# Kernel tuning notes

Measured on AMD Instinct MI355X. Metric: run time of the kernel, lower is better.

Reference implementation:

```python
import jax, jax.numpy as jnp
import numpy as np

NEG_SLOPE = 0.2  # PyG GATConv default leaky_relu slope
EPS = 1e-16


def gat_conv(x, src, dst, W, att_src, att_dst, bias, heads, concat):
    """PyG-style GATConv. x: [N, Fin]; W: [Fin, heads*C]; att_*: [heads, C].
    Edge (src j -> dst i): alpha_ij = softmax_i(leaky_relu(a_src.h_j + a_dst.h_i)).
    """
    N = x.shape[0]
    h = (x @ W).reshape(N, heads, -1)                       # [N, H, C]
    a_s = jnp.einsum('nhc,hc->nh', h, att_src)              # [N, H]
    a_d = jnp.einsum('nhc,hc->nh', h, att_dst)              # [N, H]
    e = jax.nn.leaky_relu(a_s[src] + a_d[dst], NEG_SLOPE)   # [E, H]
    # numerically stable segment softmax over incoming edges of each dst node
    e_max = jax.ops.segment_max(e, dst, num_segments=N)     # [N, H]
    e_max = jnp.where(jnp.isfinite(e_max), e_max, 0.0)      # isolated nodes
    ex = jnp.exp(e - e_max[dst])                            # [E, H]
    denom = jax.ops.segment_sum(ex, dst, num_segments=N)    # [N, H]
    alpha = ex / (denom[dst] + EPS)                         # [E, H]
    msg = alpha[:, :, None] * h[src]                        # [E, H, C]
    out = jax.ops.segment_sum(msg, dst, num_segments=N)     # [N, H, C]
    out = out.reshape(N, -1) if concat else out.mean(axis=1)
    return out + bias


def setup_inputs() -> dict:
    key = jax.random.key(0)
    ks = jax.random.split(key, 12)
    N, E = 100000, 1600000
    Fin, hidden, heads, Fout = 128, 128, 8, 64
    C1 = hidden // heads  # 16
    s = lambda f: 1.0 / np.sqrt(f)
    x = jax.random.normal(ks[0], (N, Fin), dtype=jnp.float32)
    edge_index = jax.random.randint(ks[1], (2, E), 0, N, dtype=jnp.int64)
    W1 = jax.random.normal(ks[2], (Fin, heads * C1), dtype=jnp.float32) * s(Fin)
    att_src1 = jax.random.normal(ks[3], (heads, C1), dtype=jnp.float32) * s(C1)
    att_dst1 = jax.random.normal(ks[4], (heads, C1), dtype=jnp.float32) * s(C1)
    b1 = jnp.zeros((hidden,), dtype=jnp.float32)
    W2 = jax.random.normal(ks[5], (hidden, Fout), dtype=jnp.float32) * s(hidden)
    att_src2 = jax.random.normal(ks[6], (1, Fout), dtype=jnp.float32) * s(Fout)
    att_dst2 = jax.random.normal(ks[7], (1, Fout), dtype=jnp.float32) * s(Fout)
    b2 = jnp.zeros((Fout,), dtype=jnp.float32)
    return {"x": x, "edge_index": edge_index,
            "W1": W1, "att_src1": att_src1, "att_dst1": att_dst1, "b1": b1,
            "W2": W2, "att_src2": att_src2, "att_dst2": att_dst2, "b2": b2}


def reference(x, edge_index, W1, att_src1, att_dst1, b1, W2, att_src2, att_dst2, b2):
    # eval mode: dropouts are identity
    src, dst = edge_index[0], edge_index[1]
    h = gat_conv(x, src, dst, W1, att_src1, att_dst1, b1, heads=8, concat=True)
    h = jax.nn.elu(h)
    out = gat_conv(h, src, dst, W2, att_src2, att_dst2, b2, heads=1, concat=False)
    return out
```

## Files before the change

kernel.cpp:

```cpp
#include <hip/hip_runtime.h>
#include <hip/hip_bf16.h>
#include <stdint.h>

#define SLOPE 0.2f
#define EPSV 1e-16f
#define H1W 72
#define H2W 36

#define NPB   512
#define NBMAX 256
#define NBLK1 256

typedef __attribute__((ext_vector_type(8))) short bf16x8;
typedef __attribute__((ext_vector_type(4))) float f32x4;

static __device__ __forceinline__ uint32_t cvtpk(float a, float b) {
    uint32_t r;
    asm("v_cvt_pk_bf16_f32 %0, %1, %2" : "=v"(r) : "v"(a), "v"(b));
    return r;
}
static __device__ __forceinline__ float lof(uint32_t u) { return __uint_as_float(u << 16); }
static __device__ __forceinline__ float hif(uint32_t u) { return __uint_as_float(u & 0xffff0000u); }

union FragCvt { uint4 u; bf16x8 f; };

__global__ __launch_bounds__(256) void prep_kernel(
    const float* __restrict__ W1, const float* __restrict__ W2,
    uint32_t* __restrict__ wt1hi, uint32_t* __restrict__ wt1lo,
    uint32_t* __restrict__ wt2hi, uint32_t* __restrict__ wt2lo)
{
    int t = threadIdx.x;
    if (blockIdx.x == 0) {
        for (int i = t; i < 128 * 64; i += 256) {
            int n = i >> 6, kp = i & 63;
            float w0 = W1[(2 * kp) * 128 + n], w1 = W1[(2 * kp + 1) * 128 + n];
            uint32_t h = cvtpk(w0, w1);
            wt1hi[n * 64 + kp] = h;
            wt1lo[n * 64 + kp] = cvtpk(w0 - lof(h), w1 - hif(h));
        }
    } else {
        for (int i = t; i < 64 * 64; i += 256) {
            int n = i >> 6, kp = i & 63;
            float w0 = W2[(2 * kp) * 64 + n], w1 = W2[(2 * kp + 1) * 64 + n];
            uint32_t h = cvtpk(w0, w1);
            wt2hi[n * 64 + kp] = h;
            wt2lo[n * 64 + kp] = cvtpk(w0 - lof(h), w1 - hif(h));
        }
    }
}

__global__ __launch_bounds__(256) void gemm1_mfma(
    const float* __restrict__ x,
    const uint32_t* __restrict__ wthi, const uint32_t* __restrict__ wtlo,
    const float* __restrict__ att_src, const float* __restrict__ att_dst,
    uint32_t* __restrict__ h1p, float* __restrict__ ad1, int N)
{
    __shared__ uint32_t lds[2][128 * 36];
    const int t = threadIdx.x;
    const int w = t >> 6, l = t & 63;
    const int cl = l & 15, rg = l >> 4;
    const int rowbase = blockIdx.x * 128 + w * 32;

    f32x4 zero = {0.f, 0.f, 0.f, 0.f};
    f32x4 acc[2][8];
    #pragma unroll
    for (int rt = 0; rt < 2; ++rt)
        #pragma unroll
        for (int tl = 0; tl < 8; ++tl) acc[rt][tl] = zero;

    for (int kh = 0; kh < 2; ++kh) {
        if (kh) __syncthreads();
        for (int i = t; i < 1024; i += 256) {
            int col = i >> 3, q = i & 7;
            *(uint4*)&lds[0][col * 36 + q * 4] = *(const uint4*)&wthi[col * 64 + kh * 32 + q * 4];
            *(uint4*)&lds[1][col * 36 + q * 4] = *(const uint4*)&wtlo[col * 64 + kh * 32 + q * 4];
        }
        __syncthreads();
        #pragma unroll
        for (int ks = 0; ks < 2; ++ks) {
            const int kg = kh * 64 + ks * 32 + rg * 8;
            bf16x8 ahi[2], alo[2];
            #pragma unroll
            for (int rt = 0; rt < 2; ++rt) {
                int row = rowbase + rt * 16 + cl;
                row = min(row, N - 1);
                const float* xr = x + (size_t)row * 128 + kg;
                float4 v0 = *(const float4*)xr;
                float4 v1 = *(const float4*)(xr + 4);
                uint32_t h0 = cvtpk(v0.x, v0.y), h1 = cvtpk(v0.z, v0.w);
                uint32_t h2 = cvtpk(v1.x, v1.y), h3 = cvtpk(v1.z, v1.w);
                uint32_t l0 = cvtpk(v0.x - lof(h0), v0.y - hif(h0));
                uint32_t l1 = cvtpk(v0.z - lof(h1), v0.w - hif(h1));
                uint32_t l2 = cvtpk(v1.x - lof(h2), v1.y - hif(h2));
                uint32_t l3 = cvtpk(v1.z - lof(h3), v1.w - hif(h3));
                FragCvt ch, clo;
                ch.u  = make_uint4(h0, h1, h2, h3);
                clo.u = make_uint4(l0, l1, l2, l3);
                ahi[rt] = ch.f; alo[rt] = clo.f;
            }
            #pragma unroll
            for (int tl = 0; tl < 8; ++tl) {
                const int off = (tl * 16 + cl) * 36 + ks * 16 + rg * 4;
                bf16x8 bhi = *(const bf16x8*)&lds[0][off];
                bf16x8 blo = *(const bf16x8*)&lds[1][off];
                #pragma unroll
                for (int rt = 0; rt < 2; ++rt) {
                    acc[rt][tl] = __builtin_amdgcn_mfma_f32_16x16x32_bf16(alo[rt], bhi, acc[rt][tl], 0, 0, 0);
                    acc[rt][tl] = __builtin_amdgcn_mfma_f32_16x16x32_bf16(ahi[rt], blo, acc[rt][tl], 0, 0, 0);
                    acc[rt][tl] = __builtin_amdgcn_mfma_f32_16x16x32_bf16(ahi[rt], bhi, acc[rt][tl], 0, 0, 0);
                }
            }
        }
    }

    #pragma unroll
    for (int rt = 0; rt < 2; ++rt) {
        const int rowb = rowbase + rt * 16 + rg * 4;
        #pragma unroll
        for (int tl = 0; tl < 8; ++tl) {
            f32x4 a = acc[rt][tl];
            float as_ = att_src[tl * 16 + cl], ad_ = att_dst[tl * 16 + cl];
            float s0 = a.x * as_, s1 = a.y * as_, s2 = a.z * as_, s3 = a.w * as_;
            float d0 = a.x * ad_, d1 = a.y * ad_, d2 = a.z * ad_, d3 = a.w * ad_;
            #pragma unroll
            for (int off = 1; off < 16; off <<= 1) {
                s0 += __shfl_xor(s0, off); s1 += __shfl_xor(s1, off);
                s2 += __shfl_xor(s2, off); s3 += __shfl_xor(s3, off);
                d0 += __shfl_xor(d0, off); d1 += __shfl_xor(d1, off);
                d2 += __shfl_xor(d2, off); d3 += __shfl_xor(d3, off);
            }
            float av[4] = {a.x, a.y, a.z, a.w};
            #pragma unroll
            for (int r = 0; r < 4; ++r) {
                float partner = __shfl_xor(av[r], 1);
                if (!(cl & 1)) {
                    int row = rowb + r;
                    if (row < N)
                        h1p[(size_t)row * H1W + tl * 8 + (cl >> 1)] = cvtpk(av[r], partner);
                }
            }
            if (cl == 0) {
                float sv[4] = {s0, s1, s2, s3}, dv[4] = {d0, d1, d2, d3};
                #pragma unroll
                for (int r = 0; r < 4; ++r) {
                    int row = rowb + r;
                    if (row < N) {
                        h1p[(size_t)row * H1W + 64 + tl] = __float_as_uint(sv[r]);
                        ad1[row * 8 + tl] = dv[r];
                    }
                }
            }
        }
    }
}

__global__ __launch_bounds__(256) void gemm2_mfma(
    const float* __restrict__ h,
    const uint32_t* __restrict__ wthi, const uint32_t* __restrict__ wtlo,
    const float* __restrict__ att_src, const float* __restrict__ att_dst,
    uint32_t* __restrict__ h2p, float* __restrict__ ad2, int N)
{
    __shared__ uint32_t lds[2][64 * 36];
    const int t = threadIdx.x;
    const int w = t >> 6, l = t & 63;
    const int cl = l & 15, rg = l >> 4;
    const int rowbase = blockIdx.x * 128 + w * 32;

    f32x4 zero = {0.f, 0.f, 0.f, 0.f};
    f32x4 acc[2][4];
    #pragma unroll
    for (int rt = 0; rt < 2; ++rt)
        #pragma unroll
        for (int tl = 0; tl < 4; ++tl) acc[rt][tl] = zero;

    for (int kh = 0; kh < 2; ++kh) {
        if (kh) __syncthreads();
        for (int i = t; i < 512; i += 256) {
            int col = i >> 3, q = i & 7;
            *(uint4*)&lds[0][col * 36 + q * 4] = *(const uint4*)&wthi[col * 64 + kh * 32 + q * 4];
            *(uint4*)&lds[1][col * 36 + q * 4] = *(const uint4*)&wtlo[col * 64 + kh * 32 + q * 4];
        }
        __syncthreads();
        #pragma unroll
        for (int ks = 0; ks < 2; ++ks) {
            const int kg = kh * 64 + ks * 32 + rg * 8;
            bf16x8 ahi[2], alo[2];
            #pragma unroll
            for (int rt = 0; rt < 2; ++rt) {
                int row = rowbase + rt * 16 + cl;
                row = min(row, N - 1);
                const float* xr = h + (size_t)row * 128 + kg;
                float4 v0 = *(const float4*)xr;
                float4 v1 = *(const float4*)(xr + 4);
                uint32_t h0 = cvtpk(v0.x, v0.y), h1 = cvtpk(v0.z, v0.w);
                uint32_t h2 = cvtpk(v1.x, v1.y), h3 = cvtpk(v1.z, v1.w);
                uint32_t l0 = cvtpk(v0.x - lof(h0), v0.y - hif(h0));
                uint32_t l1 = cvtpk(v0.z - lof(h1), v0.w - hif(h1));
                uint32_t l2 = cvtpk(v1.x - lof(h2), v1.y - hif(h2));
                uint32_t l3 = cvtpk(v1.z - lof(h3), v1.w - hif(h3));
                FragCvt ch, clo;
                ch.u  = make_uint4(h0, h1, h2, h3);
                clo.u = make_uint4(l0, l1, l2, l3);
                ahi[rt] = ch.f; alo[rt] = clo.f;
            }
            #pragma unroll
            for (int tl = 0; tl < 4; ++tl) {
                const int off = (tl * 16 + cl) * 36 + ks * 16 + rg * 4;
                bf16x8 bhi = *(const bf16x8*)&lds[0][off];
                bf16x8 blo = *(const bf16x8*)&lds[1][off];
                #pragma unroll
                for (int rt = 0; rt < 2; ++rt) {
                    acc[rt][tl] = __builtin_amdgcn_mfma_f32_16x16x32_bf16(alo[rt], bhi, acc[rt][tl], 0, 0, 0);
                    acc[rt][tl] = __builtin_amdgcn_mfma_f32_16x16x32_bf16(ahi[rt], blo, acc[rt][tl], 0, 0, 0);
                    acc[rt][tl] = __builtin_amdgcn_mfma_f32_16x16x32_bf16(ahi[rt], bhi, acc[rt][tl], 0, 0, 0);
                }
            }
        }
    }

    #pragma unroll
    for (int rt = 0; rt < 2; ++rt) {
        const int rowb = rowbase + rt * 16 + rg * 4;
        float s0 = 0.f, s1 = 0.f, s2 = 0.f, s3 = 0.f;
        float d0 = 0.f, d1 = 0.f, d2 = 0.f, d3 = 0.f;
        #pragma unroll
        for (int tl = 0; tl < 4; ++tl) {
            f32x4 a = acc[rt][tl];
            float as_ = att_src[tl * 16 + cl], ad_ = att_dst[tl * 16 + cl];
            s0 += a.x * as_; s1 += a.y * as_; s2 += a.z * as_; s3 += a.w * as_;
            d0 += a.x * ad_; d1 += a.y * ad_; d2 += a.z * ad_; d3 += a.w * ad_;
            float av[4] = {a.x, a.y, a.z, a.w};
            #pragma unroll
            for (int r = 0; r < 4; ++r) {
                float partner = __shfl_xor(av[r], 1);
                if (!(cl & 1)) {
                    int row = rowb + r;
                    if (row < N)
                        h2p[(size_t)row * H2W + tl * 8 + (cl >> 1)] = cvtpk(av[r], partner);
                }
            }
        }
        #pragma unroll
        for (int off = 1; off < 16; off <<= 1) {
            s0 += __shfl_xor(s0, off); s1 += __shfl_xor(s1, off);
            s2 += __shfl_xor(s2, off); s3 += __shfl_xor(s3, off);
            d0 += __shfl_xor(d0, off); d1 += __shfl_xor(d1, off);
            d2 += __shfl_xor(d2, off); d3 += __shfl_xor(d3, off);
        }
        if (cl == 0) {
            float sv[4] = {s0, s1, s2, s3}, dv[4] = {d0, d1, d2, d3};
            #pragma unroll
            for (int r = 0; r < 4; ++r) {
                int row = rowb + r;
                if (row < N) {
                    h2p[(size_t)row * H2W + 32] = __float_as_uint(sv[r]);
                    ad2[row] = dv[r];
                }
            }
        }
    }
}

__global__ __launch_bounds__(256) void p1_count_kernel(
    const int* __restrict__ ei, int* __restrict__ pbh, int E, int NB, int chunk)
{
    __shared__ int hist[NBMAX];
    int t = threadIdx.x;
    if (t < NB) hist[t] = 0;
    __syncthreads();
    int e0 = blockIdx.x * chunk;
    int e1 = min(E, e0 + chunk);
    for (int e = e0 + t; e < e1; e += 256)
        atomicAdd(&hist[ei[E + e] >> 9], 1);
    __syncthreads();
    if (t < NB) pbh[t * NBLK1 + blockIdx.x] = hist[t];
}

__global__ __launch_bounds__(256) void p1_scan_kernel(
    int* __restrict__ pbh, int* __restrict__ bucket_base, int NB, int E)
{
    __shared__ int ps[256];
    int t = threadIdx.x;
    int s = 0;
    if (t < NB) {
        const int* row = &pbh[t * NBLK1];
        for (int b = 0; b < NBLK1; ++b) s += row[b];
    }
    ps[t] = s; __syncthreads();
    for (int off = 1; off < 256; off <<= 1) {
        int add = (t >= off) ? ps[t - off] : 0;
        __syncthreads();
        ps[t] += add;
        __syncthreads();
    }
    int base = ps[t] - s;
    if (t < NB) {
        bucket_base[t] = base;
        int* row = &pbh[t * NBLK1];
        int run = base;
        for (int b = 0; b < NBLK1; ++b) {
            int c = row[b];
            row[b] = run;
            run += c;
        }
    }
    if (t == 0) bucket_base[NB] = E;
}

__global__ __launch_bounds__(256) void p1_place_kernel(
    const int* __restrict__ ei, const int* __restrict__ pbh,
    uint32_t* __restrict__ staging, int E, int NB, int chunk)
{
    __shared__ int lcur[NBMAX];
    int t = threadIdx.x;
    if (t < NB) lcur[t] = pbh[t * NBLK1 + blockIdx.x];
    __syncthreads();
    int e0 = blockIdx.x * chunk;
    int e1 = min(E, e0 + chunk);
    for (int e = e0 + t; e < e1; e += 256) {
        int s = ei[e], d = ei[E + e];
        int b = d >> 9;
        int p = atomicAdd(&lcur[b], 1);
        staging[p] = ((uint32_t)s << 9) | (uint32_t)(d & 511);
    }
}

__global__ __launch_bounds__(256) void p2_build_kernel(
    const uint32_t* __restrict__ staging, const int* __restrict__ bucket_base,
    int* __restrict__ row_start, int* __restrict__ sorted_src, int N, int E, int NB)
{
    __shared__ int cnt[NPB];
    __shared__ int ofs[NPB];
    __shared__ int ps[256];
    int b = blockIdx.x, t = threadIdx.x;
    int base = bucket_base[b], end = bucket_base[b + 1];
    cnt[t] = 0; cnt[t + 256] = 0;
    __syncthreads();
    for (int i = base + t; i < end; i += 256)
        atomicAdd(&cnt[staging[i] & 511], 1);
    __syncthreads();
    int c0 = cnt[2 * t], c1 = cnt[2 * t + 1];
    int p = c0 + c1;
    ps[t] = p; __syncthreads();
    for (int off = 1; off < 256; off <<= 1) {
        int add = (t >= off) ? ps[t - off] : 0;
        __syncthreads();
        ps[t] += add;
        __syncthreads();
    }
    int pex = ps[t] - p;
    ofs[2 * t] = pex;
    ofs[2 * t + 1] = pex + c0;
    __syncthreads();
    int node0 = b * NPB;
    #pragma unroll
    for (int i = t; i < NPB; i += 256) {
        int node = node0 + i;
        if (node < N) row_start[node] = base + ofs[i];
    }
    if (b == NB - 1 && t == 0) row_start[N] = E;
    __syncthreads();
    for (int i = base + t; i < end; i += 256) {
        uint32_t v = staging[i];
        int nl = v & 511;
        int pos = base + atomicAdd(&ofs[nl], 1);
        sorted_src[pos] = (int)(v >> 9);
    }
}

__global__ __launch_bounds__(256) void gather1_kernel(
    const int* __restrict__ row_start, const int* __restrict__ sorted_src,
    const float* __restrict__ ad1, const uint32_t* __restrict__ h1p,
    const float* __restrict__ b1, float* __restrict__ hbuf, int N)
{
    int node = blockIdx.x * 4 + (threadIdx.x >> 6);
    if (node >= N) return;
    int lane = threadIdx.x & 63;
    int cw = lane;
    int hh = lane >> 3;
    int wh = lane & 7;
    int r0 = row_start[node], r1 = row_start[node + 1];
    float ad_w = ad1[node * 8 + wh];
    const uint32_t* pch = h1p + cw;
    float acc0 = 0.0f, acc1 = 0.0f, den = 0.0f;

    for (int j = r0; j < r1; j += 8) {
        int jw = j + (lane >> 3);
        bool vw = jw < r1;
        int sw = sorted_src[vw ? jw : r0];
        int swoff = sw * H1W;
        float av = __uint_as_float(h1p[swoff + 64 + wh]);
        float ev = av + ad_w;
        ev = ev > 0.0f ? ev : SLOPE * ev;
        float w = vw ? __expf(ev) : 0.0f;

        #pragma unroll
        for (int k = 0; k < 8; ++k) {
            float wk   = __shfl(w,     k * 8 + hh, 64);
            int   offk = __shfl(swoff, k * 8 + wh, 64);
            uint32_t hv = pch[offk];
            den += wk;
            acc0 = fmaf(wk, __uint_as_float(hv << 16), acc0);
            acc1 = fmaf(wk, __uint_as_float(hv & 0xffff0000u), acc1);
        }
    }
    float inv = 1.0f / (den + EPSV);
    float v0 = acc0 * inv + b1[cw * 2];
    float v1 = acc1 * inv + b1[cw * 2 + 1];
    v0 = v0 > 0.0f ? v0 : expm1f(v0);
    v1 = v1 > 0.0f ? v1 : expm1f(v1);
    *(float2*)&hbuf[(size_t)node * 128 + cw * 2] = make_float2(v0, v1);
}

__global__ __launch_bounds__(256) void gather2_kernel(
    const int* __restrict__ row_start, const int* __restrict__ sorted_src,
    const float* __restrict__ ad2, const uint32_t* __restrict__ h2p,
    const float* __restrict__ b2, float* __restrict__ out, int N)
{
    int node = blockIdx.x * 8 + (threadIdx.x >> 5);
    if (node >= N) return;
    int lane = threadIdx.x & 31;
    int cw = lane;
    int r0 = row_start[node], r1 = row_start[node + 1];
    float ad = ad2[node];
    const uint32_t* pch = h2p + cw;
    float acc0 = 0.0f, acc1 = 0.0f, den = 0.0f;

    for (int j = r0; j < r1; j += 8) {
        int jw = j + (lane & 7);
        bool vw = jw < r1;
        int sw = sorted_src[vw ? jw : r0];
        int swoff = sw * H2W;
        float av = __uint_as_float(h2p[swoff + 32]);
        float ev = av + ad;
        ev = ev > 0.0f ? ev : SLOPE * ev;
        float w = vw ? __expf(ev) : 0.0f;

        #pragma unroll
        for (int k = 0; k < 8; ++k) {
            float wk   = __shfl(w,     k, 32);
            int   offk = __shfl(swoff, k, 32);
            uint32_t hv = pch[offk];
            den += wk;
            acc0 = fmaf(wk, __uint_as_float(hv << 16), acc0);
            acc1 = fmaf(wk, __uint_as_float(hv & 0xffff0000u), acc1);
        }
    }
    float inv = 1.0f / (den + EPSV);
    *(float2*)&out[(size_t)node * 64 + cw * 2] =
        make_float2(acc0 * inv + b2[cw * 2], acc1 * inv + b2[cw * 2 + 1]);
}

extern "C" void kernel_launch(void* const* d_in, const int* in_sizes, int n_in,
                              void* d_out, int out_size, void* d_ws, size_t ws_size,
                              hipStream_t stream)
{
    const int N = in_sizes[0] / 128;
    const int E = in_sizes[1] / 2;
    const int NB = (N + NPB - 1) / NPB;
    const int chunk = (E + NBLK1 - 1) / NBLK1;

    const float* x        = (const float*)d_in[0];
    const int*   ei       = (const int*)  d_in[1];
    const float* W1       = (const float*)d_in[2];
    const float* att_src1 = (const float*)d_in[3];
    const float* att_dst1 = (const float*)d_in[4];
    const float* b1       = (const float*)d_in[5];
    const float* W2       = (const float*)d_in[6];
    const float* att_src2 = (const float*)d_in[7];
    const float* att_dst2 = (const float*)d_in[8];
    const float* b2       = (const float*)d_in[9];
    float* out = (float*)d_out;

    uint32_t* h1p  = (uint32_t*)d_ws;
    float* hbuf    = (float*)(h1p + (size_t)N * H1W);
    float* ad1     = hbuf + (size_t)N * 128;
    float* ad2     = ad1  + (size_t)N * 8;
    int* row_start   = (int*)(ad2 + N);
    int* bucket_base = row_start + (N + 1);
    int* pbh         = bucket_base + (NB + 1);
    int* sorted_src  = pbh + NB * NBLK1;
    uint32_t* staging = (uint32_t*)(sorted_src + E);
    uint32_t* wt1hi = staging + E;
    uint32_t* wt1lo = wt1hi + 128 * 64;
    uint32_t* wt2hi = wt1lo + 128 * 64;
    uint32_t* wt2lo = wt2hi + 64 * 64;
    uint32_t* h2p   = h1p;

    prep_kernel<<<2, 256, 0, stream>>>(W1, W2, wt1hi, wt1lo, wt2hi, wt2lo);

    p1_count_kernel<<<NBLK1, 256, 0, stream>>>(ei, pbh, E, NB, chunk);
    p1_scan_kernel <<<1, 256, 0, stream>>>(pbh, bucket_base, NB, E);
    p1_place_kernel<<<NBLK1, 256, 0, stream>>>(ei, pbh, staging, E, NB, chunk);
    p2_build_kernel<<<NB, 256, 0, stream>>>(staging, bucket_base, row_start, sorted_src, N, E, NB);

    gemm1_mfma<<<(N + 127) / 128, 256, 0, stream>>>(x, wt1hi, wt1lo, att_src1, att_dst1, h1p, ad1, N);
    gather1_kernel<<<(N + 3) / 4, 256, 0, stream>>>(row_start, sorted_src, ad1, h1p, b1, hbuf, N);

    gemm2_mfma<<<(N + 127) / 128, 256, 0, stream>>>(hbuf, wt2hi, wt2lo, att_src2, att_dst2, h2p, ad2, N);
    gather2_kernel<<<(N + 7) / 8, 256, 0, stream>>>(row_start, sorted_src, ad2, h2p, b2, out, N);
}
```

Measured before the change: 281.1 us.

## Restructure GAT gather kernels with prefetching, wider loads and split-edge lanes

Both gather kernels now software-pipeline the neighbour index and attention-score loads two edge groups ahead, so their latency overlaps the feature accumulation. Each lane loads 8 bytes (four bf16 channels), and the two wave halves process alternate edges, which halves the inner-loop trip count. Partial sums are combined with cross-lane shuffles at the end. Nodes with no incoming edges take an early exit that writes only the bias. The cost is extra registers, the shuffle reductions, and idle half-waves during the final write.

Result: no change. 280.1 us (-0.4%).

```diff
diff --git a/kernel.cpp b/kernel.cpp
--- a/kernel.cpp
+++ b/kernel.cpp
@@ -375,41 +375,83 @@
 {
     int node = blockIdx.x * 4 + (threadIdx.x >> 6);
     if (node >= N) return;
-    int lane = threadIdx.x & 63;
-    int cw = lane;
-    int hh = lane >> 3;
-    int wh = lane & 7;
+    const int l   = threadIdx.x & 63;
+    const int wh  = l & 7;
+    const int eA  = l >> 3;
+    const int c4  = l & 31;
+    const int par = l >> 5;
+    const int hB  = c4 >> 2;
+
     int r0 = row_start[node], r1 = row_start[node + 1];
-    float ad_w = ad1[node * 8 + wh];
-    const uint32_t* pch = h1p + cw;
-    float acc0 = 0.0f, acc1 = 0.0f, den = 0.0f;
+
+    if (r0 == r1) {
+        if (l < 32) {
+            float4 bv = *(const float4*)&b1[c4 * 4];
+            bv.x = bv.x > 0.f ? bv.x : expm1f(bv.x);
+            bv.y = bv.y > 0.f ? bv.y : expm1f(bv.y);
+            bv.z = bv.z > 0.f ? bv.z : expm1f(bv.z);
+            bv.w = bv.w > 0.f ? bv.w : expm1f(bv.w);
+            *(float4*)&hbuf[(size_t)node * 128 + c4 * 4] = bv;
+        }
+        return;
+    }
+
+    float adw = ad1[node * 8 + wh];
+    float acc0 = 0.f, acc1 = 0.f, acc2 = 0.f, acc3 = 0.f, den = 0.f;
+
+    int jw = r0 + eA;
+    int sw0 = sorted_src[jw < r1 ? jw : r0] * H1W;
+    int j1 = r0 + 8 + eA;
+    int sw1 = sorted_src[j1 < r1 ? j1 : r0] * H1W;
+    float av0 = __uint_as_float(h1p[sw0 + 64 + wh]);
 
     for (int j = r0; j < r1; j += 8) {
-        int jw = j + (lane >> 3);
-        bool vw = jw < r1;
-        int sw = sorted_src[vw ? jw : r0];
-        int swoff = sw * H1W;
-        float av = __uint_as_float(h1p[swoff + 64 + wh]);
-        float ev = av + ad_w;
-        ev = ev > 0.0f ? ev : SLOPE * ev;
-        float w = vw ? __expf(ev) : 0.0f;
-
-        #pragma unroll
-        for (int k = 0; k < 8; ++k) {
-            float wk   = __shfl(w,     k * 8 + hh, 64);
-            int   offk = __shfl(swoff, k * 8 + wh, 64);
-            uint32_t hv = pch[offk];
-            den += wk;
-            acc0 = fmaf(wk, __uint_as_float(hv << 16), acc0);
-            acc1 = fmaf(wk, __uint_as_float(hv & 0xffff0000u), acc1);
-        }
-    }
-    float inv = 1.0f / (den + EPSV);
-    float v0 = acc0 * inv + b1[cw * 2];
-    float v1 = acc1 * inv + b1[cw * 2 + 1];
-    v0 = v0 > 0.0f ? v0 : expm1f(v0);
-    v1 = v1 > 0.0f ? v1 : expm1f(v1);
-    *(float2*)&hbuf[(size_t)node * 128 + cw * 2] = make_float2(v0, v1);
+        int jn = j + 16 + eA;
+        int swn = sorted_src[jn < r1 ? jn : r0] * H1W;
+        float avn = __uint_as_float(h1p[sw1 + 64 + wh]);
+
+        float ev = av0 + adw;
+        ev = ev > 0.f ? ev : SLOPE * ev;
+        float w = (j + eA) < r1 ? __expf(ev) : 0.f;
+        den += w;
+
+        #pragma unroll
+        for (int k = 0; k < 4; ++k) {
+            int eidx = 2 * k + par;
+            float wk  = __shfl(w,   eidx * 8 + hB, 64);
+            int   ofk = __shfl(sw0, eidx * 8,      64);
+            uint2 hv = *(const uint2*)&h1p[ofk + 2 * c4];
+            acc0 = fmaf(wk, lof(hv.x), acc0);
+            acc1 = fmaf(wk, hif(hv.x), acc1);
+            acc2 = fmaf(wk, lof(hv.y), acc2);
+            acc3 = fmaf(wk, hif(hv.y), acc3);
+        }
+        sw0 = sw1; sw1 = swn; av0 = avn;
+    }
+
+    den += __shfl_xor(den, 8, 64);
+    den += __shfl_xor(den, 16, 64);
+    den += __shfl_xor(den, 32, 64);
+    float dB = __shfl(den, hB, 64);
+
+    acc0 += __shfl_xor(acc0, 32, 64);
+    acc1 += __shfl_xor(acc1, 32, 64);
+    acc2 += __shfl_xor(acc2, 32, 64);
+    acc3 += __shfl_xor(acc3, 32, 64);
+
+    if (l < 32) {
+        float inv = 1.0f / (dB + EPSV);
+        float4 bv = *(const float4*)&b1[c4 * 4];
+        float v0 = acc0 * inv + bv.x;
+        float v1 = acc1 * inv + bv.y;
+        float v2 = acc2 * inv + bv.z;
+        float v3 = acc3 * inv + bv.w;
+        v0 = v0 > 0.f ? v0 : expm1f(v0);
+        v1 = v1 > 0.f ? v1 : expm1f(v1);
+        v2 = v2 > 0.f ? v2 : expm1f(v2);
+        v3 = v3 > 0.f ? v3 : expm1f(v3);
+        *(float4*)&hbuf[(size_t)node * 128 + c4 * 4] = make_float4(v0, v1, v2, v3);
+    }
 }
 
 __global__ __launch_bounds__(256) void gather2_kernel(
@@ -419,36 +461,69 @@
 {
     int node = blockIdx.x * 8 + (threadIdx.x >> 5);
     if (node >= N) return;
-    int lane = threadIdx.x & 31;
-    int cw = lane;
+    const int l   = threadIdx.x & 31;
+    const int eA  = l & 7;
+    const int c4  = l & 15;
+    const int par = (l >> 4) & 1;
+
     int r0 = row_start[node], r1 = row_start[node + 1];
+
+    if (r0 == r1) {
+        if (l < 16) {
+            float4 bv = *(const float4*)&b2[c4 * 4];
+            *(float4*)&out[(size_t)node * 64 + c4 * 4] = bv;
+        }
+        return;
+    }
+
     float ad = ad2[node];
-    const uint32_t* pch = h2p + cw;
-    float acc0 = 0.0f, acc1 = 0.0f, den = 0.0f;
+    float acc0 = 0.f, acc1 = 0.f, acc2 = 0.f, acc3 = 0.f, den = 0.f;
+
+    int jw = r0 + eA;
+    int sw0 = sorted_src[jw < r1 ? jw : r0] * H2W;
+    int j1 = r0 + 8 + eA;
+    int sw1 = sorted_src[j1 < r1 ? j1 : r0] * H2W;
+    float av0 = __uint_as_float(h2p[sw0 + 32]);
 
     for (int j = r0; j < r1; j += 8) {
-        int jw = j + (lane & 7);
-        bool vw = jw < r1;
-        int sw = sorted_src[vw ? jw : r0];
-        int swoff = sw * H2W;
-        float av = __uint_as_float(h2p[swoff + 32]);
-        float ev = av + ad;
-        ev = ev > 0.0f ? ev : SLOPE * ev;
-        float w = vw ? __expf(ev) : 0.0f;
-
-        #pragma unroll
-        for (int k = 0; k < 8; ++k) {
-            float wk   = __shfl(w,     k, 32);
-            int   offk = __shfl(swoff, k, 32);
-            uint32_t hv = pch[offk];
-            den += wk;
-            acc0 = fmaf(wk, __uint_as_float(hv << 16), acc0);
-            acc1 = fmaf(wk, __uint_as_float(hv & 0xffff0000u), acc1);
-        }
-    }
-    float inv = 1.0f / (den + EPSV);
-    *(float2*)&out[(size_t)node * 64 + cw * 2] =
-        make_float2(acc0 * inv + b2[cw * 2], acc1 * inv + b2[cw * 2 + 1]);
+        int jn = j + 16 + eA;
+        int swn = sorted_src[jn < r1 ? jn : r0] * H2W;
+        float avn = __uint_as_float(h2p[sw1 + 32]);
+
+        float ev = av0 + ad;
+        ev = ev > 0.f ? ev : SLOPE * ev;
+        float w = (j + eA) < r1 ? __expf(ev) : 0.f;
+        den += w;
+
+        #pragma unroll
+        for (int k = 0; k < 4; ++k) {
+            int eidx = 2 * k + par;
+            float wk  = __shfl(w,   eidx, 32);
+            int   ofk = __shfl(sw0, eidx, 32);
+            uint2 hv = *(const uint2*)&h2p[ofk + 2 * c4];
+            acc0 = fmaf(wk, lof(hv.x), acc0);
+            acc1 = fmaf(wk, hif(hv.x), acc1);
+            acc2 = fmaf(wk, lof(hv.y), acc2);
+            acc3 = fmaf(wk, hif(hv.y), acc3);
+        }
+        sw0 = sw1; sw1 = swn; av0 = avn;
+    }
+
+    den += __shfl_xor(den, 1, 32);
+    den += __shfl_xor(den, 2, 32);
+    den += __shfl_xor(den, 4, 32);
+    acc0 += __shfl_xor(acc0, 16, 32);
+    acc1 += __shfl_xor(acc1, 16, 32);
+    acc2 += __shfl_xor(acc2, 16, 32);
+    acc3 += __shfl_xor(acc3, 16, 32);
+
+    if (l < 16) {
+        float inv = 1.0f / (den + EPSV);
+        float4 bv = *(const float4*)&b2[c4 * 4];
+        *(float4*)&out[(size_t)node * 64 + c4 * 4] =
+            make_float4(acc0 * inv + bv.x, acc1 * inv + bv.y,
+                        acc2 * inv + bv.z, acc3 * inv + bv.w);
+    }
 }
 
 extern "C" void kernel_launch(void* const* d_in, const int* in_sizes, int n_in,
```

## Split gathered features into per-head fp16 slabs and restructure gather kernels

Applied to the files above, without the earlier changes.

Node features are now stored as per-head (or per-slice) fp16 tables with separate transposed attention-score arrays, instead of interleaved bf16 rows with the scores appended. The gather kernels are reorganised so that each block handles one head or slice across 32 nodes, which keeps each table slab small enough to stay cache-resident across blocks. Neighbour indices are software-prefetched two iterations ahead, accumulation uses mixed-precision FMA on packed fp16 values, and log2(e) is folded into the attention vectors so exp2 can replace exp. The trade-offs are that fp16 has less range than bf16 and the same edge list is re-read once per head.

Measured after the change: 400.8 us. 1.43x slower.

```diff
diff --git a/kernel.cpp b/kernel.cpp
--- a/kernel.cpp
+++ b/kernel.cpp
@@ -1,11 +1,11 @@
 #include <hip/hip_runtime.h>
 #include <hip/hip_bf16.h>
+#include <hip/hip_fp16.h>
 #include <stdint.h>
 
 #define SLOPE 0.2f
 #define EPSV 1e-16f
-#define H1W 72
-#define H2W 36
+#define LOG2E 1.44269504f
 
 #define NPB   512
 #define NBMAX 256
@@ -21,6 +21,18 @@
 }
 static __device__ __forceinline__ float lof(uint32_t u) { return __uint_as_float(u << 16); }
 static __device__ __forceinline__ float hif(uint32_t u) { return __uint_as_float(u & 0xffff0000u); }
+
+static __device__ __forceinline__ uint32_t pkf16(float a, float b) {
+    auto r = __builtin_amdgcn_cvt_pkrtz(a, b);
+    return __builtin_bit_cast(uint32_t, r);
+}
+
+static __device__ __forceinline__ void fmix_lo(float& acc, uint32_t h2, float w) {
+    asm("v_fma_mix_f32 %0, %1, %2, %0 op_sel_hi:[1,0,0]" : "+v"(acc) : "v"(h2), "v"(w));
+}
+static __device__ __forceinline__ void fmix_hi(float& acc, uint32_t h2, float w) {
+    asm("v_fma_mix_f32 %0, %1, %2, %0 op_sel:[1,0,0] op_sel_hi:[1,0,0]" : "+v"(acc) : "v"(h2), "v"(w));
+}
 
 union FragCvt { uint4 u; bf16x8 f; };
 
@@ -53,7 +65,9 @@
     const float* __restrict__ x,
     const uint32_t* __restrict__ wthi, const uint32_t* __restrict__ wtlo,
     const float* __restrict__ att_src, const float* __restrict__ att_dst,
-    uint32_t* __restrict__ h1p, float* __restrict__ ad1, int N)
+    uint32_t* __restrict__ h1s,
+    float* __restrict__ as1t, float* __restrict__ ad1t,
+    int N)
 {
     __shared__ uint32_t lds[2][128 * 36];
     const int t = threadIdx.x;
@@ -119,7 +133,7 @@
         #pragma unroll
         for (int tl = 0; tl < 8; ++tl) {
             f32x4 a = acc[rt][tl];
-            float as_ = att_src[tl * 16 + cl], ad_ = att_dst[tl * 16 + cl];
+            float as_ = att_src[tl * 16 + cl] * LOG2E, ad_ = att_dst[tl * 16 + cl] * LOG2E;
             float s0 = a.x * as_, s1 = a.y * as_, s2 = a.z * as_, s3 = a.w * as_;
             float d0 = a.x * ad_, d1 = a.y * ad_, d2 = a.z * ad_, d3 = a.w * ad_;
             #pragma unroll
@@ -136,7 +150,7 @@
                 if (!(cl & 1)) {
                     int row = rowb + r;
                     if (row < N)
-                        h1p[(size_t)row * H1W + tl * 8 + (cl >> 1)] = cvtpk(av[r], partner);
+                        h1s[((size_t)tl * N + row) * 8 + (cl >> 1)] = pkf16(av[r], partner);
                 }
             }
             if (cl == 0) {
@@ -145,8 +159,8 @@
                 for (int r = 0; r < 4; ++r) {
                     int row = rowb + r;
                     if (row < N) {
-                        h1p[(size_t)row * H1W + 64 + tl] = __float_as_uint(sv[r]);
-                        ad1[row * 8 + tl] = dv[r];
+                        as1t[(size_t)tl * N + row] = sv[r];
+                        ad1t[(size_t)tl * N + row] = dv[r];
                     }
                 }
             }
@@ -158,7 +172,9 @@
     const float* __restrict__ h,
     const uint32_t* __restrict__ wthi, const uint32_t* __restrict__ wtlo,
     const float* __restrict__ att_src, const float* __restrict__ att_dst,
-    uint32_t* __restrict__ h2p, float* __restrict__ ad2, int N)
+    uint32_t* __restrict__ h2s,
+    float* __restrict__ as2t, float* __restrict__ ad2t,
+    int N)
 {
     __shared__ uint32_t lds[2][64 * 36];
     const int t = threadIdx.x;
@@ -226,7 +242,7 @@
         #pragma unroll
         for (int tl = 0; tl < 4; ++tl) {
             f32x4 a = acc[rt][tl];
-            float as_ = att_src[tl * 16 + cl], ad_ = att_dst[tl * 16 + cl];
+            float as_ = att_src[tl * 16 + cl] * LOG2E, ad_ = att_dst[tl * 16 + cl] * LOG2E;
             s0 += a.x * as_; s1 += a.y * as_; s2 += a.z * as_; s3 += a.w * as_;
             d0 += a.x * ad_; d1 += a.y * ad_; d2 += a.z * ad_; d3 += a.w * ad_;
             float av[4] = {a.x, a.y, a.z, a.w};
@@ -235,8 +251,10 @@
                 float partner = __shfl_xor(av[r], 1);
                 if (!(cl & 1)) {
                     int row = rowb + r;
-                    if (row < N)
-                        h2p[(size_t)row * H2W + tl * 8 + (cl >> 1)] = cvtpk(av[r], partner);
+                    if (row < N) {
+                        int s = tl * 2 + (cl >> 3);
+                        h2s[((size_t)s * N + row) * 4 + ((cl >> 1) & 3)] = pkf16(av[r], partner);
+                    }
                 }
             }
         }
@@ -253,8 +271,8 @@
             for (int r = 0; r < 4; ++r) {
                 int row = rowb + r;
                 if (row < N) {
-                    h2p[(size_t)row * H2W + 32] = __float_as_uint(sv[r]);
-                    ad2[row] = dv[r];
+                    as2t[row] = sv[r];
+                    ad2t[row] = dv[r];
                 }
             }
         }
@@ -370,85 +388,151 @@
 
 __global__ __launch_bounds__(256) void gather1_kernel(
     const int* __restrict__ row_start, const int* __restrict__ sorted_src,
-    const float* __restrict__ ad1, const uint32_t* __restrict__ h1p,
-    const float* __restrict__ b1, float* __restrict__ hbuf, int N)
-{
-    int node = blockIdx.x * 4 + (threadIdx.x >> 6);
+    const uint32_t* __restrict__ h1s, const float* __restrict__ as1t,
+    const float* __restrict__ ad1t, const float* __restrict__ b1,
+    float* __restrict__ hbuf, int N)
+{
+    const int head = blockIdx.x & 7;
+    const int lane = threadIdx.x & 63;
+    const int l3   = lane & 7;
+    const int node = (blockIdx.x >> 3) * 32 + (threadIdx.x >> 6) * 8 + (lane >> 3);
     if (node >= N) return;
-    int lane = threadIdx.x & 63;
-    int cw = lane;
-    int hh = lane >> 3;
-    int wh = lane & 7;
+
+    const uint32_t* tab = h1s + (size_t)head * N * 8;
+    const float*    asl = as1t + (size_t)head * N;
+    const float adw = ad1t[(size_t)head * N + node];
     int r0 = row_start[node], r1 = row_start[node + 1];
-    float ad_w = ad1[node * 8 + wh];
-    const uint32_t* pch = h1p + cw;
-    float acc0 = 0.0f, acc1 = 0.0f, den = 0.0f;
-
-    for (int j = r0; j < r1; j += 8) {
-        int jw = j + (lane >> 3);
-        bool vw = jw < r1;
-        int sw = sorted_src[vw ? jw : r0];
-        int swoff = sw * H1W;
-        float av = __uint_as_float(h1p[swoff + 64 + wh]);
-        float ev = av + ad_w;
-        ev = ev > 0.0f ? ev : SLOPE * ev;
-        float w = vw ? __expf(ev) : 0.0f;
-
-        #pragma unroll
-        for (int k = 0; k < 8; ++k) {
-            float wk   = __shfl(w,     k * 8 + hh, 64);
-            int   offk = __shfl(swoff, k * 8 + wh, 64);
-            uint32_t hv = pch[offk];
-            den += wk;
-            acc0 = fmaf(wk, __uint_as_float(hv << 16), acc0);
-            acc1 = fmaf(wk, __uint_as_float(hv & 0xffff0000u), acc1);
-        }
-    }
-    float inv = 1.0f / (den + EPSV);
-    float v0 = acc0 * inv + b1[cw * 2];
-    float v1 = acc1 * inv + b1[cw * 2 + 1];
-    v0 = v0 > 0.0f ? v0 : expm1f(v0);
-    v1 = v1 > 0.0f ? v1 : expm1f(v1);
-    *(float2*)&hbuf[(size_t)node * 128 + cw * 2] = make_float2(v0, v1);
+
+    float acc[8] = {0.f, 0.f, 0.f, 0.f, 0.f, 0.f, 0.f, 0.f};
+    float den = 0.f;
+
+    if (r0 < r1) {
+        int jw = r0 + l3;
+        int sw0 = sorted_src[jw < r1 ? jw : r0];
+        int j1 = r0 + 8 + l3;
+        int sw1 = sorted_src[j1 < r1 ? j1 : r0];
+        float av0 = asl[sw0];
+
+        for (int j = r0; j < r1; j += 8) {
+            int jn = j + 16 + l3;
+            int swn = sorted_src[jn < r1 ? jn : r0];
+            float avn = asl[sw1];
+
+            float ev = av0 + adw;
+            ev = ev > 0.f ? ev : SLOPE * ev;
+            float w = (j + l3) < r1 ? exp2f(ev) : 0.f;
+            den += w;
+
+            #pragma unroll
+            for (int p = 0; p < 2; ++p) {
+                int srcl = (lane & 56) | (p * 4 + (l3 >> 1));
+                float wk = __shfl(w, srcl, 64);
+                int   sk = __shfl(sw0, srcl, 64);
+                uint4 hv = *(const uint4*)(tab + (size_t)sk * 8 + (l3 & 1) * 4);
+                fmix_lo(acc[0], hv.x, wk); fmix_hi(acc[1], hv.x, wk);
+                fmix_lo(acc[2], hv.y, wk); fmix_hi(acc[3], hv.y, wk);
+                fmix_lo(acc[4], hv.z, wk); fmix_hi(acc[5], hv.z, wk);
+                fmix_lo(acc[6], hv.w, wk); fmix_hi(acc[7], hv.w, wk);
+            }
+            sw0 = sw1; sw1 = swn; av0 = avn;
+        }
+    }
+
+    den += __shfl_xor(den, 1, 64);
+    den += __shfl_xor(den, 2, 64);
+    den += __shfl_xor(den, 4, 64);
+    #pragma unroll
+    for (int i = 0; i < 8; ++i) {
+        acc[i] += __shfl_xor(acc[i], 2, 64);
+        acc[i] += __shfl_xor(acc[i], 4, 64);
+    }
+
+    if (l3 < 2) {
+        float inv = 1.0f / (den + EPSV);
+        const int cb = head * 16 + l3 * 8;
+        float4 b0 = *(const float4*)&b1[cb];
+        float4 b4 = *(const float4*)&b1[cb + 4];
+        float v0 = acc[0] * inv + b0.x, v1 = acc[1] * inv + b0.y;
+        float v2 = acc[2] * inv + b0.z, v3 = acc[3] * inv + b0.w;
+        float v4 = acc[4] * inv + b4.x, v5 = acc[5] * inv + b4.y;
+        float v6 = acc[6] * inv + b4.z, v7 = acc[7] * inv + b4.w;
+        v0 = v0 > 0.f ? v0 : expm1f(v0); v1 = v1 > 0.f ? v1 : expm1f(v1);
+        v2 = v2 > 0.f ? v2 : expm1f(v2); v3 = v3 > 0.f ? v3 : expm1f(v3);
+        v4 = v4 > 0.f ? v4 : expm1f(v4); v5 = v5 > 0.f ? v5 : expm1f(v5);
+        v6 = v6 > 0.f ? v6 : expm1f(v6); v7 = v7 > 0.f ? v7 : expm1f(v7);
+        *(float4*)&hbuf[(size_t)node * 128 + cb]     = make_float4(v0, v1, v2, v3);
+        *(float4*)&hbuf[(size_t)node * 128 + cb + 4] = make_float4(v4, v5, v6, v7);
+    }
 }
 
 __global__ __launch_bounds__(256) void gather2_kernel(
     const int* __restrict__ row_start, const int* __restrict__ sorted_src,
-    const float* __restrict__ ad2, const uint32_t* __restrict__ h2p,
-    const float* __restrict__ b2, float* __restrict__ out, int N)
-{
-    int node = blockIdx.x * 8 + (threadIdx.x >> 5);
+    const uint32_t* __restrict__ h2s, const float* __restrict__ as2t,
+    const float* __restrict__ ad2t, const float* __restrict__ b2,
+    float* __restrict__ out, int N)
+{
+    const int sl   = blockIdx.x & 7;
+    const int lane = threadIdx.x & 63;
+    const int l3   = lane & 7;
+    const int node = (blockIdx.x >> 3) * 32 + (threadIdx.x >> 6) * 8 + (lane >> 3);
     if (node >= N) return;
-    int lane = threadIdx.x & 31;
-    int cw = lane;
+
+    const uint32_t* tab = h2s + (size_t)sl * N * 4;
+    const float adw = ad2t[node];
     int r0 = row_start[node], r1 = row_start[node + 1];
-    float ad = ad2[node];
-    const uint32_t* pch = h2p + cw;
-    float acc0 = 0.0f, acc1 = 0.0f, den = 0.0f;
-
-    for (int j = r0; j < r1; j += 8) {
-        int jw = j + (lane & 7);
-        bool vw = jw < r1;
-        int sw = sorted_src[vw ? jw : r0];
-        int swoff = sw * H2W;
-        float av = __uint_as_float(h2p[swoff + 32]);
-        float ev = av + ad;
-        ev = ev > 0.0f ? ev : SLOPE * ev;
-        float w = vw ? __expf(ev) : 0.0f;
-
-        #pragma unroll
-        for (int k = 0; k < 8; ++k) {
-            float wk   = __shfl(w,     k, 32);
-            int   offk = __shfl(swoff, k, 32);
-            uint32_t hv = pch[offk];
-            den += wk;
-            acc0 = fmaf(wk, __uint_as_float(hv << 16), acc0);
-            acc1 = fmaf(wk, __uint_as_float(hv & 0xffff0000u), acc1);
-        }
-    }
-    float inv = 1.0f / (den + EPSV);
-    *(float2*)&out[(size_t)node * 64 + cw * 2] =
-        make_float2(acc0 * inv + b2[cw * 2], acc1 * inv + b2[cw * 2 + 1]);
+
+    float acc[8] = {0.f, 0.f, 0.f, 0.f, 0.f, 0.f, 0.f, 0.f};
+    float den = 0.f;
+
+    if (r0 < r1) {
+        int jw = r0 + l3;
+        int sw0 = sorted_src[jw < r1 ? jw : r0];
+        int j1 = r0 + 8 + l3;
+        int sw1 = sorted_src[j1 < r1 ? j1 : r0];
+        float av0 = as2t[sw0];
+
+        for (int j = r0; j < r1; j += 8) {
+            int jn = j + 16 + l3;
+            int swn = sorted_src[jn < r1 ? jn : r0];
+            float avn = as2t[sw1];
+
+            float ev = av0 + adw;
+            ev = ev > 0.f ? ev : SLOPE * ev;
+            float w = (j + l3) < r1 ? exp2f(ev) : 0.f;
+            den += w;
+
+            uint4 hv = *(const uint4*)(tab + (size_t)sw0 * 4);
+            fmix_lo(acc[0], hv.x, w); fmix_hi(acc[1], hv.x, w);
+            fmix_lo(acc[2], hv.y, w); fmix_hi(acc[3], hv.y, w);
+            fmix_lo(acc[4], hv.z, w); fmix_hi(acc[5], hv.z, w);
+            fmix_lo(acc[6], hv.w, w); fmix_hi(acc[7], hv.w, w);
+
+            sw0 = sw1; sw1 = swn; av0 = avn;
+        }
+    }
+
+    den += __shfl_xor(den, 1, 64);
+    den += __shfl_xor(den, 2, 64);
+    den += __shfl_xor(den, 4, 64);
+    #pragma unroll
+    for (int i = 0; i < 8; ++i) {
+        acc[i] += __shfl_xor(acc[i], 1, 64);
+        acc[i] += __shfl_xor(acc[i], 2, 64);
+        acc[i] += __shfl_xor(acc[i], 4, 64);
+    }
+
+    if (l3 == 0) {
+        float inv = 1.0f / (den + EPSV);
+        const int cb = sl * 8;
+        float4 b0 = *(const float4*)&b2[cb];
+        float4 b4 = *(const float4*)&b2[cb + 4];
+        *(float4*)&out[(size_t)node * 64 + cb] =
+            make_float4(acc[0] * inv + b0.x, acc[1] * inv + b0.y,
+                        acc[2] * inv + b0.z, acc[3] * inv + b0.w);
+        *(float4*)&out[(size_t)node * 64 + cb + 4] =
+            make_float4(acc[4] * inv + b4.x, acc[5] * inv + b4.y,
+                        acc[6] * inv + b4.z, acc[7] * inv + b4.w);
+    }
 }
 
 extern "C" void kernel_launch(void* const* d_in, const int* in_sizes, int n_in,
@@ -472,11 +556,11 @@
     const float* b2       = (const float*)d_in[9];
     float* out = (float*)d_out;
 
-    uint32_t* h1p  = (uint32_t*)d_ws;
-    float* hbuf    = (float*)(h1p + (size_t)N * H1W);
-    float* ad1     = hbuf + (size_t)N * 128;
-    float* ad2     = ad1  + (size_t)N * 8;
-    int* row_start   = (int*)(ad2 + N);
+    uint32_t* h1s  = (uint32_t*)d_ws;
+    float* as1t    = (float*)(h1s + (size_t)64 * N);
+    float* ad1t    = as1t + (size_t)8 * N;
+    float* hbuf    = ad1t + (size_t)8 * N;
+    int* row_start   = (int*)(hbuf + (size_t)128 * N);
     int* bucket_base = row_start + (N + 1);
     int* pbh         = bucket_base + (NB + 1);
     int* sorted_src  = pbh + NB * NBLK1;
@@ -485,7 +569,9 @@
     uint32_t* wt1lo = wt1hi + 128 * 64;
     uint32_t* wt2hi = wt1lo + 128 * 64;
     uint32_t* wt2lo = wt2hi + 64 * 64;
-    uint32_t* h2p   = h1p;
+    uint32_t* h2s   = h1s;
+    float* as2t     = as1t;
+    float* ad2t     = ad1t;
 
     prep_kernel<<<2, 256, 0, stream>>>(W1, W2, wt1hi, wt1lo, wt2hi, wt2lo);
 
@@ -494,9 +580,13 @@
     p1_place_kernel<<<NBLK1, 256, 0, stream>>>(ei, pbh, staging, E, NB, chunk);
     p2_build_kernel<<<NB, 256, 0, stream>>>(staging, bucket_base, row_start, sorted_src, N, E, NB);
 
-    gemm1_mfma<<<(N + 127) / 128, 256, 0, stream>>>(x, wt1hi, wt1lo, att_src1, att_dst1, h1p, ad1, N);
-    gather1_kernel<<<(N + 3) / 4, 256, 0, stream>>>(row_start, sorted_src, ad1, h1p, b1, hbuf, N);
-
-    gemm2_mfma<<<(N + 127) / 128, 256, 0, stream>>>(hbuf, wt2hi, wt2lo, att_src2, att_dst2, h2p, ad2, N);
-    gather2_kernel<<<(N + 7) / 8, 256, 0, stream>>>(row_start, sorted_src, ad2, h2p, b2, out, N);
-}
+    const int gblocks = ((N + 31) / 32) * 8;
+
+    gemm1_mfma<<<(N + 127) / 128, 256, 0, stream>>>(x, wt1hi, wt1lo, att_src1, att_dst1,
+                                                    h1s, as1t, ad1t, N);
+    gather1_kernel<<<gblocks, 256, 0, stream>>>(row_start, sorted_src, h1s, as1t, ad1t, b1, hbuf, N);
+
+    gemm2_mfma<<<(N + 127) / 128, 256, 0, stream>>>(hbuf, wt2hi, wt2lo, att_src2, att_dst2,
+                                                    h2s, as2t, ad2t, N);
+    gather2_kernel<<<gblocks, 256, 0, stream>>>(row_start, sorted_src, h2s, as2t, ad2t, b2, out, N);
+}
```
